# Kernel tuning notes

Measured on AMD Instinct MI355X. Metric: run time of the kernel, lower is better.

Reference implementation:

```python
import jax, jax.numpy as jnp
import numpy as np

NUM_USERS = 100000
NUM_ITEMS = 100000
D = 128
L = 8
FV = 64
FH = 64
B = 8192
FC_IN = FV * D + FH * L  # 8704


def setup_inputs() -> dict:
    key = jax.random.key(0)
    ks = jax.random.split(key, 16)
    s = 0.05  # weight scale for sane magnitudes
    return {
        "user_id": jax.random.randint(ks[0], (B,), 0, NUM_USERS),
        "seq_L": jax.random.randint(ks[1], (B, L), 0, NUM_ITEMS),
        "item_id": jax.random.randint(ks[2], (B,), 0, NUM_ITEMS),
        "Q": jax.random.normal(ks[3], (NUM_ITEMS, D), jnp.float32) * s,
        "P": jax.random.normal(ks[4], (NUM_USERS, D), jnp.float32) * s,
        "Qp": jax.random.normal(ks[5], (NUM_ITEMS, 2 * D), jnp.float32) * s,
        "b_item": jax.random.normal(ks[6], (NUM_ITEMS,), jnp.float32) * s,
        "Wv": jax.random.normal(ks[7], (FV, L), jnp.float32) * s,
        "bv": jax.random.normal(ks[8], (FV,), jnp.float32) * s,
        "Wh": jax.random.normal(ks[9], (L, FH, L, D), jnp.float32) * s,
        "bh": jax.random.normal(ks[10], (L, FH), jnp.float32) * s,
        "Wfc": jax.random.normal(ks[11], (D, FC_IN), jnp.float32) * s,
        "bfc": jax.random.normal(ks[12], (D,), jnp.float32) * s,
    }


def reference(user_id, seq_L, item_id, Q, P, Qp, b_item, Wv, bv, Wh, bh, Wfc, bfc):
    # seq embeddings: [B, L, D]
    x = Q[seq_L]
    # vertical conv: kernel (L,1) -> out [B, Fv, D], then relu + flatten
    out_v = jax.nn.relu(jnp.einsum("bld,fl->bfd", x, Wv) + bv[None, :, None])
    out_v = out_v.reshape(out_v.shape[0], FV * D)  # [B, Fv*D]
    # horizontal conv blocks h = 1..L (static loop over kernel heights)
    h_feats = []
    for h in range(1, L + 1):
        w = Wh[h - 1, :, :h, :]  # [Fh, h, D]
        # sliding windows over sequence: [B, L-h+1, h, D]
        win = jnp.stack([x[:, j : j + h] for j in range(L - h + 1)], axis=1)
        o = jnp.einsum("bjhd,fhd->bjf", win, w) + bh[h - 1]  # [B, L-h+1, Fh]
        h_feats.append(jnp.max(jax.nn.relu(o), axis=1))  # [B, Fh]
    out_h = jnp.concatenate(h_feats, axis=1)  # [B, Fh*L]
    combined = jnp.concatenate([out_v, out_h], axis=1)  # [B, Fv*D + Fh*L]
    # (dropout p=0 / inference -> identity)
    z = jax.nn.relu(combined @ Wfc.T + bfc)  # [B, D]
    x2 = jnp.concatenate([z, P[user_id]], axis=1)  # [B, 2D]
    score = jnp.einsum("bd,bd->b", x2, Qp[item_id]) + b_item[item_id]
    return score
```

## Files before the change

kernel.cpp:

```cpp
#include <hip/hip_runtime.h>
#include <hip/hip_bf16.h>
#include <cstdint>
#include <cstddef>

typedef short bf16x8 __attribute__((ext_vector_type(8)));
typedef short bf16x4 __attribute__((ext_vector_type(4)));
typedef float f32x4  __attribute__((ext_vector_type(4)));

#define MFMA16(A, B, C) __builtin_amdgcn_mfma_f32_16x16x32_bf16(A, B, C, 0, 0, 0)

constexpr int XSTR = 1032;
constexpr int BSTR = 520;
constexpr size_t WS_FC   = (size_t)2176 * 1024;
constexpr size_t WS_BOTH = WS_FC + (size_t)576 * 1024;

__device__ __forceinline__ unsigned short f2bf(float x) {
    unsigned u = __float_as_uint(x);
    unsigned r = u + 0x7fffu + ((u >> 16) & 1u);
    return (unsigned short)(r >> 16);
}
__device__ __forceinline__ float bf2f(unsigned short h) {
    return __uint_as_float(((unsigned)h) << 16);
}
__device__ __forceinline__ unsigned pkbf(float a, float b) {
    __hip_bfloat162 h = __float22bfloat162_rn(make_float2(a, b));
    return *reinterpret_cast<unsigned*>(&h);
}
__device__ __forceinline__ bf16x8 load8_f32(const float* __restrict__ s) {
    float4 a = *(const float4*)s;
    float4 b = *(const float4*)(s + 4);
    bf16x8 r;
    r[0]=(short)f2bf(a.x); r[1]=(short)f2bf(a.y); r[2]=(short)f2bf(a.z); r[3]=(short)f2bf(a.w);
    r[4]=(short)f2bf(b.x); r[5]=(short)f2bf(b.y); r[6]=(short)f2bf(b.z); r[7]=(short)f2bf(b.w);
    return r;
}

template<int MODE>
__device__ __forceinline__ bf16x8 fc_bfrag(const unsigned short* __restrict__ wfcb,
                                           const float* __restrict__ Wfc,
                                           int kg, int ntile, int lane)
{
    if constexpr (MODE >= 1) {
        return *(const bf16x8*)(wfcb + (((size_t)(kg * 8 + ntile)) << 9) + lane * 8);
    } else {
        const float* s = Wfc + (size_t)(ntile * 16 + (lane & 15)) * 8704
                             + kg * 32 + (lane >> 4) * 8;
        return load8_f32(s);
    }
}
template<int MODE>
__device__ __forceinline__ bf16x8 wh_bfrag(const unsigned short* __restrict__ whb,
                                           const float* __restrict__ Wh,
                                           int H, int kstep, int ntile, int lane)
{
    if constexpr (MODE == 2) {
        return *(const bf16x8*)(whb +
            (((size_t)(8 * H * (H - 1) + kstep * 4 + ntile)) << 9) + lane * 8);
    } else {
        const int k = kstep * 32 + (lane >> 4) * 8;
        const float* s = Wh + ((((size_t)(H - 1) * 64 + ntile * 16 + (lane & 15)) * 8
                               + (k >> 7)) * 128 + (k & 127));
        return load8_f32(s);
    }
}

__global__ __launch_bounds__(256)
void caser_prep(const float* __restrict__ Wfc, const float* __restrict__ Wh,
                unsigned short* __restrict__ wfcb, unsigned short* __restrict__ whb,
                int nfrag)
{
    const int tid = blockIdx.x * 256 + threadIdx.x;
    const int lane = tid & 63, frag = tid >> 6;
    if (frag >= nfrag) return;
    if (frag < 2176) {
        const int kg = frag >> 3, nt = frag & 7;
        bf16x8 v = fc_bfrag<0>(nullptr, Wfc, kg, nt, lane);
        *(bf16x8*)(wfcb + ((size_t)frag << 9) + lane * 8) = v;
    } else {
        const int f2 = frag - 2176;
        int h = 1;
        while (f2 >= 8 * h * (h + 1)) ++h;
        const int fl = f2 - 8 * h * (h - 1);
        const int nt = fl & 3, kstep = fl >> 2;
        bf16x8 v = wh_bfrag<0>(nullptr, Wh, h, kstep, nt, lane);
        *(bf16x8*)(whb + ((size_t)f2 << 9) + lane * 8) = v;
    }
}

template<int H, int PP, int MODE>
__device__ __forceinline__ void hconv_compute(
    const unsigned short* __restrict__ xs,
    const unsigned short* __restrict__ whb, const float* __restrict__ Wh,
    const float* __restrict__ bh,
    int m, int nt4, int lane, int laneA, float mx[4])
{
    constexpr int NJ = 9 - H;
    constexpr int NJS = (PP == 0) ? ((NJ + 1) / 2) : (NJ / 2);
    if constexpr (NJS > 0) {
        f32x4 C[NJS] = {};
        const unsigned short* xbase = xs + m * 16 * XSTR + laneA;
        #pragma unroll
        for (int kstep = 0; kstep < 4 * H; ++kstep) {
            const int hp = kstep >> 2, d0 = (kstep & 3) * 32;
            bf16x8 B = wh_bfrag<MODE>(whb, Wh, H, kstep, nt4, lane);
            #pragma unroll
            for (int idx = 0; idx < NJS; ++idx) {
                const int j = PP + 2 * idx;
                bf16x8 A = *(const bf16x8*)(xbase + (j + hp) * 128 + d0);
                C[idx] = MFMA16(A, B, C[idx]);
            }
        }
        const float bhv = bh[(H - 1) * 64 + nt4 * 16 + (lane & 15)];
        #pragma unroll
        for (int idx = 0; idx < NJS; ++idx)
            #pragma unroll
            for (int r = 0; r < 4; ++r)
                mx[r] = fmaxf(mx[r], fmaxf(C[idx][r] + bhv, 0.f));
    }
}

template<int H, int MODE>
__device__ __forceinline__ void hstep(
    const unsigned short* __restrict__ xs, unsigned short* __restrict__ feat,
    float* __restrict__ cand,
    const unsigned short* __restrict__ whb, const float* __restrict__ Wh,
    const float* __restrict__ bh,
    int t, int lane, int laneA, int hm, int hn4, int pj)
{
    float mx[4] = {};
    if (pj == 0) hconv_compute<H, 0, MODE>(xs, whb, Wh, bh, hm, hn4, lane, laneA, mx);
    else         hconv_compute<H, 1, MODE>(xs, whb, Wh, bh, hm, hn4, lane, laneA, mx);
    #pragma unroll
    for (int r = 0; r < 4; ++r)
        cand[pj * 2176 + (hm * 16 + (lane >> 4) * 4 + r) * 68 +
             hn4 * 16 + (lane & 15)] = mx[r];
    __syncthreads();
    {
        const int s = t >> 5, f0 = (t & 31) * 2;
        float a0 = fmaxf(cand[s * 68 + f0],     cand[2176 + s * 68 + f0]);
        float a1 = fmaxf(cand[s * 68 + f0 + 1], cand[2176 + s * 68 + f0 + 1]);
        *(unsigned*)(feat + s * BSTR + (H - 1) * 64 + f0) = pkbf(a0, a1);
    }
    __syncthreads();
}

template<int MODE>
__global__ __launch_bounds__(1024, 1)
void caser_main(const int* __restrict__ user_id,
                const int* __restrict__ seq,
                const int* __restrict__ item_id,
                const float* __restrict__ Q,
                const float* __restrict__ Pmat,
                const float* __restrict__ Qp,
                const float* __restrict__ b_item,
                const float* __restrict__ Wv,
                const float* __restrict__ bv,
                const float* __restrict__ Wh,
                const float* __restrict__ bh,
                const float* __restrict__ Wfc,
                const float* __restrict__ bfc,
                const unsigned short* __restrict__ wfcb,
                const unsigned short* __restrict__ whb,
                float* __restrict__ out)
{
    __shared__ unsigned short xs[32 * XSTR];
    __shared__ unsigned short fbuf[2 * 32 * BSTR];
    __shared__ float cand[2 * 32 * 68];
    __shared__ float wv_s[576];

    const int t = threadIdx.x;
    const int lane = t & 63;
    const int w = t >> 6;
    const int b0 = blockIdx.x * 32;
    const int laneA = (lane & 15) * XSTR + (lane >> 4) * 8;
    const int laneB = (lane & 15) * BSTR + (lane >> 4) * 8;
    const int kh = w & 3, ng = w >> 2;
    const int hm = w & 1, hn4 = (w >> 1) & 3, pj = (w >> 3) & 1;

    if (t < 576) wv_s[t] = (t < 512) ? Wv[t] : bv[t - 512];
    #pragma unroll
    for (int k = 0; k < 8; ++k) {
        const int idx = t + k * 1024;
        const int i = idx & 31;
        const int l = (idx >> 5) & 7;
        const int s = idx >> 8;
        const int it = seq[(b0 + s) * 8 + l];
        float4 v = *(const float4*)(Q + (size_t)it * 128 + i * 4);
        uint2 pk;
        pk.x = pkbf(v.x, v.y);
        pk.y = pkbf(v.z, v.w);
        *(uint2*)(xs + s * XSTR + l * 128 + i * 4) = pk;
    }
    __syncthreads();

    const int sv = t & 31, dq = t >> 5;
    float xr[8][4];
    #pragma unroll
    for (int l = 0; l < 8; ++l) {
        bf16x4 v = *(const bf16x4*)(xs + sv * XSTR + l * 128 + dq * 4);
        #pragma unroll
        for (int i = 0; i < 4; ++i) xr[l][i] = bf2f((unsigned short)v[i]);
    }

    f32x4 FCC[2][2] = {};

    uint2 vc[4];
    #define VCONV_HALF(hc_, dst_)                                              \
        {                                                                      \
            _Pragma("unroll")                                                  \
            for (int fl = 0; fl < 4; ++fl) {                                   \
                const int f = (hc_) * 4 + fl;                                  \
                const float bvv = wv_s[512 + f];                               \
                float acc[4];                                                  \
                _Pragma("unroll")                                              \
                for (int i = 0; i < 4; ++i) acc[i] = bvv;                      \
                _Pragma("unroll")                                              \
                for (int l = 0; l < 8; ++l) {                                  \
                    const float wl = wv_s[f * 8 + l];                          \
                    _Pragma("unroll")                                          \
                    for (int i = 0; i < 4; ++i)                                \
                        acc[i] = fmaf(xr[l][i], wl, acc[i]);                   \
                }                                                              \
                dst_[fl].x = pkbf(fmaxf(acc[0], 0.f), fmaxf(acc[1], 0.f));     \
                dst_[fl].y = pkbf(fmaxf(acc[2], 0.f), fmaxf(acc[3], 0.f));     \
            }                                                                  \
        }
    #define VSTORE(buf_)                                                       \
        {                                                                      \
            unsigned short* fb = fbuf + (buf_) * (32 * BSTR);                  \
            _Pragma("unroll")                                                  \
            for (int fl = 0; fl < 4; ++fl)                                     \
                *(uint2*)(fb + sv * BSTR + fl * 128 + dq * 4) = vc[fl];        \
        }

    VCONV_HALF(0, vc);
    VSTORE(0);
    __syncthreads();

    #pragma unroll 2
    for (int hc = 0; hc < 16; ++hc) {
        uint2 nxt[4];
        if (hc < 15) VCONV_HALF(hc + 1, nxt);
        {
            const unsigned short* fb = fbuf + (hc & 1) * (32 * BSTR);
            #pragma unroll
            for (int ks = 0; ks < 4; ++ks) {
                const int kl = kh * 4 + ks;
                const int kg = hc * 16 + kl;
                bf16x8 B0 = fc_bfrag<MODE>(wfcb, Wfc, kg, ng * 2,     lane);
                bf16x8 B1 = fc_bfrag<MODE>(wfcb, Wfc, kg, ng * 2 + 1, lane);
                bf16x8 A0 = *(const bf16x8*)(fb + laneB + kl * 32);
                bf16x8 A1 = *(const bf16x8*)(fb + 16 * BSTR + laneB + kl * 32);
                FCC[0][0] = MFMA16(A0, B0, FCC[0][0]);
                FCC[0][1] = MFMA16(A0, B1, FCC[0][1]);
                FCC[1][0] = MFMA16(A1, B0, FCC[1][0]);
                FCC[1][1] = MFMA16(A1, B1, FCC[1][1]);
            }
        }
        if (hc < 15) {
            #pragma unroll
            for (int fl = 0; fl < 4; ++fl) vc[fl] = nxt[fl];
            VSTORE((hc + 1) & 1);
        }
        __syncthreads();
    }
    #undef VCONV_HALF
    #undef VSTORE

    unsigned short* feat = fbuf;
    hstep<1, MODE>(xs, feat, cand, whb, Wh, bh, t, lane, laneA, hm, hn4, pj);
    hstep<2, MODE>(xs, feat, cand, whb, Wh, bh, t, lane, laneA, hm, hn4, pj);
    hstep<3, MODE>(xs, feat, cand, whb, Wh, bh, t, lane, laneA, hm, hn4, pj);
    hstep<4, MODE>(xs, feat, cand, whb, Wh, bh, t, lane, laneA, hm, hn4, pj);
    hstep<5, MODE>(xs, feat, cand, whb, Wh, bh, t, lane, laneA, hm, hn4, pj);
    hstep<6, MODE>(xs, feat, cand, whb, Wh, bh, t, lane, laneA, hm, hn4, pj);
    hstep<7, MODE>(xs, feat, cand, whb, Wh, bh, t, lane, laneA, hm, hn4, pj);
    hstep<8, MODE>(xs, feat, cand, whb, Wh, bh, t, lane, laneA, hm, hn4, pj);

    #pragma unroll
    for (int kgi = 0; kgi < 4; ++kgi) {
        const int kloc = kh * 4 + kgi;
        const int kg = 256 + kloc;
        bf16x8 B0 = fc_bfrag<MODE>(wfcb, Wfc, kg, ng * 2,     lane);
        bf16x8 B1 = fc_bfrag<MODE>(wfcb, Wfc, kg, ng * 2 + 1, lane);
        bf16x8 A0 = *(const bf16x8*)(feat + laneB + kloc * 32);
        bf16x8 A1 = *(const bf16x8*)(feat + 16 * BSTR + laneB + kloc * 32);
        FCC[0][0] = MFMA16(A0, B0, FCC[0][0]);
        FCC[0][1] = MFMA16(A0, B1, FCC[0][1]);
        FCC[1][0] = MFMA16(A1, B0, FCC[1][0]);
        FCC[1][1] = MFMA16(A1, B1, FCC[1][1]);
    }

    float* zbuf4 = (float*)xs;
    #pragma unroll
    for (int m = 0; m < 2; ++m)
        #pragma unroll
        for (int nt = 0; nt < 2; ++nt)
            #pragma unroll
            for (int r = 0; r < 4; ++r)
                zbuf4[kh * (32 * 132) + (m * 16 + (lane >> 4) * 4 + r) * 132 +
                      ng * 32 + nt * 16 + (lane & 15)] = FCC[m][nt][r];
    __syncthreads();
    {
        const int s = t >> 5, l32 = t & 31, o0 = l32 * 4;
        const int b = b0 + s;
        const int item = item_id[b];
        const int user = user_id[b];
        const float* qp = Qp + (size_t)item * 256;
        const float* pu = Pmat + (size_t)user * 128;
        float acc2 = 0.f;
        #pragma unroll
        for (int i = 0; i < 4; ++i) {
            float z = zbuf4[s * 132 + o0 + i]
                    + zbuf4[1 * (32 * 132) + s * 132 + o0 + i]
                    + zbuf4[2 * (32 * 132) + s * 132 + o0 + i]
                    + zbuf4[3 * (32 * 132) + s * 132 + o0 + i]
                    + bfc[o0 + i];
            z = fmaxf(z, 0.f);
            acc2 = fmaf(z, qp[o0 + i], acc2);
        }
        #pragma unroll
        for (int i = 0; i < 4; ++i)
            acc2 = fmaf(pu[o0 + i], qp[128 + o0 + i], acc2);
        acc2 += __shfl_xor(acc2, 1, 32);
        acc2 += __shfl_xor(acc2, 2, 32);
        acc2 += __shfl_xor(acc2, 4, 32);
        acc2 += __shfl_xor(acc2, 8, 32);
        acc2 += __shfl_xor(acc2, 16, 32);
        if (l32 == 0) out[b] = acc2 + b_item[item];
    }
}

extern "C" void kernel_launch(void* const* d_in, const int* in_sizes, int n_in,
                              void* d_out, int out_size, void* d_ws, size_t ws_size,
                              hipStream_t stream)
{
    const int*   user_id = (const int*)  d_in[0];
    const int*   seq     = (const int*)  d_in[1];
    const int*   item_id = (const int*)  d_in[2];
    const float* Q       = (const float*)d_in[3];
    const float* Pmat    = (const float*)d_in[4];
    const float* Qp      = (const float*)d_in[5];
    const float* b_item  = (const float*)d_in[6];
    const float* Wv      = (const float*)d_in[7];
    const float* bv      = (const float*)d_in[8];
    const float* Wh      = (const float*)d_in[9];
    const float* bh      = (const float*)d_in[10];
    const float* Wfc     = (const float*)d_in[11];
    const float* bfc     = (const float*)d_in[12];
    float* out = (float*)d_out;

    unsigned short* wfcb = (unsigned short*)d_ws;
    unsigned short* whb  = wfcb + WS_FC / 2;

    if (ws_size >= WS_BOTH) {
        hipLaunchKernelGGL(caser_prep, dim3(688), dim3(256), 0, stream,
                           Wfc, Wh, wfcb, whb, 2752);
        hipLaunchKernelGGL((caser_main<2>), dim3(256), dim3(1024), 0, stream,
                           user_id, seq, item_id, Q, Pmat, Qp, b_item,
                           Wv, bv, Wh, bh, Wfc, bfc, wfcb, whb, out);
    } else if (ws_size >= WS_FC) {
        hipLaunchKernelGGL(caser_prep, dim3(544), dim3(256), 0, stream,
                           Wfc, Wh, wfcb, whb, 2176);
        hipLaunchKernelGGL((caser_main<1>), dim3(256), dim3(1024), 0, stream,
                           user_id, seq, item_id, Q, Pmat, Qp, b_item,
                           Wv, bv, Wh, bh, Wfc, bfc, wfcb, whb, out);
    } else {
        hipLaunchKernelGGL((caser_main<0>), dim3(256), dim3(1024), 0, stream,
                           user_id, seq, item_id, Q, Pmat, Qp, b_item,
                           Wv, bv, Wh, bh, Wfc, bfc,
                           (const unsigned short*)nullptr, (const unsigned short*)nullptr, out);
    }
}
```

Baseline: 85.87 us.

## Prefetch FC weight fragments a chunk ahead and double-buffer hconv candidate buffers

FC weight B-fragments are now loaded into registers one chunk ahead of their use, so their global latency overlaps the current chunk's MFMAs instead of stalling them. The vertical conv for the next chunk moves after the MFMAs, and the loop unroll drops to 1. The horizontal conv steps alternate between two candidate buffers, which removes one barrier per step, and the tail FC fragment loads are issued before the final sync. This raises register pressure and reuses part of fbuf as scratch, which is only safe if the lifetimes of those regions do not overlap.

```diff
diff --git a/kernel.cpp b/kernel.cpp
--- a/kernel.cpp
+++ b/kernel.cpp
@@ -122,7 +122,7 @@
 template<int H, int MODE>
 __device__ __forceinline__ void hstep(
     const unsigned short* __restrict__ xs, unsigned short* __restrict__ feat,
-    float* __restrict__ cand,
+    float* __restrict__ candc,
     const unsigned short* __restrict__ whb, const float* __restrict__ Wh,
     const float* __restrict__ bh,
     int t, int lane, int laneA, int hm, int hn4, int pj)
@@ -132,16 +132,15 @@
     else         hconv_compute<H, 1, MODE>(xs, whb, Wh, bh, hm, hn4, lane, laneA, mx);
     #pragma unroll
     for (int r = 0; r < 4; ++r)
-        cand[pj * 2176 + (hm * 16 + (lane >> 4) * 4 + r) * 68 +
-             hn4 * 16 + (lane & 15)] = mx[r];
+        candc[pj * 2176 + (hm * 16 + (lane >> 4) * 4 + r) * 68 +
+              hn4 * 16 + (lane & 15)] = mx[r];
     __syncthreads();
     {
         const int s = t >> 5, f0 = (t & 31) * 2;
-        float a0 = fmaxf(cand[s * 68 + f0],     cand[2176 + s * 68 + f0]);
-        float a1 = fmaxf(cand[s * 68 + f0 + 1], cand[2176 + s * 68 + f0 + 1]);
+        float a0 = fmaxf(candc[s * 68 + f0],     candc[2176 + s * 68 + f0]);
+        float a1 = fmaxf(candc[s * 68 + f0 + 1], candc[2176 + s * 68 + f0 + 1]);
         *(unsigned*)(feat + s * BSTR + (H - 1) * 64 + f0) = pkbf(a0, a1);
     }
-    __syncthreads();
 }
 
 template<int MODE>
@@ -205,7 +204,7 @@
     f32x4 FCC[2][2] = {};
 
     uint2 vc[4];
-    #define VCONV_HALF(hc_, dst_)                                              \
+    #define VCONV_HALF(hc_)                                                    \
         {                                                                      \
             _Pragma("unroll")                                                  \
             for (int fl = 0; fl < 4; ++fl) {                                   \
@@ -221,8 +220,8 @@
                     for (int i = 0; i < 4; ++i)                                \
                         acc[i] = fmaf(xr[l][i], wl, acc[i]);                   \
                 }                                                              \
-                dst_[fl].x = pkbf(fmaxf(acc[0], 0.f), fmaxf(acc[1], 0.f));     \
-                dst_[fl].y = pkbf(fmaxf(acc[2], 0.f), fmaxf(acc[3], 0.f));     \
+                vc[fl].x = pkbf(fmaxf(acc[0], 0.f), fmaxf(acc[1], 0.f));       \
+                vc[fl].y = pkbf(fmaxf(acc[2], 0.f), fmaxf(acc[3], 0.f));       \
             }                                                                  \
         }
     #define VSTORE(buf_)                                                       \
@@ -233,33 +232,40 @@
                 *(uint2*)(fb + sv * BSTR + fl * 128 + dq * 4) = vc[fl];        \
         }
 
-    VCONV_HALF(0, vc);
+    bf16x8 BF0[4], BF1[4];
+    #pragma unroll
+    for (int ks = 0; ks < 4; ++ks) {
+        const int kg = kh * 4 + ks;
+        BF0[ks] = fc_bfrag<MODE>(wfcb, Wfc, kg, ng * 2,     lane);
+        BF1[ks] = fc_bfrag<MODE>(wfcb, Wfc, kg, ng * 2 + 1, lane);
+    }
+    VCONV_HALF(0);
     VSTORE(0);
     __syncthreads();
 
-    #pragma unroll 2
+    #pragma unroll 1
     for (int hc = 0; hc < 16; ++hc) {
-        uint2 nxt[4];
-        if (hc < 15) VCONV_HALF(hc + 1, nxt);
         {
             const unsigned short* fb = fbuf + (hc & 1) * (32 * BSTR);
             #pragma unroll
             for (int ks = 0; ks < 4; ++ks) {
                 const int kl = kh * 4 + ks;
-                const int kg = hc * 16 + kl;
-                bf16x8 B0 = fc_bfrag<MODE>(wfcb, Wfc, kg, ng * 2,     lane);
-                bf16x8 B1 = fc_bfrag<MODE>(wfcb, Wfc, kg, ng * 2 + 1, lane);
                 bf16x8 A0 = *(const bf16x8*)(fb + laneB + kl * 32);
                 bf16x8 A1 = *(const bf16x8*)(fb + 16 * BSTR + laneB + kl * 32);
-                FCC[0][0] = MFMA16(A0, B0, FCC[0][0]);
-                FCC[0][1] = MFMA16(A0, B1, FCC[0][1]);
-                FCC[1][0] = MFMA16(A1, B0, FCC[1][0]);
-                FCC[1][1] = MFMA16(A1, B1, FCC[1][1]);
+                FCC[0][0] = MFMA16(A0, BF0[ks], FCC[0][0]);
+                FCC[0][1] = MFMA16(A0, BF1[ks], FCC[0][1]);
+                FCC[1][0] = MFMA16(A1, BF0[ks], FCC[1][0]);
+                FCC[1][1] = MFMA16(A1, BF1[ks], FCC[1][1]);
             }
         }
         if (hc < 15) {
             #pragma unroll
-            for (int fl = 0; fl < 4; ++fl) vc[fl] = nxt[fl];
+            for (int ks = 0; ks < 4; ++ks) {
+                const int kg = (hc + 1) * 16 + kh * 4 + ks;
+                BF0[ks] = fc_bfrag<MODE>(wfcb, Wfc, kg, ng * 2,     lane);
+                BF1[ks] = fc_bfrag<MODE>(wfcb, Wfc, kg, ng * 2 + 1, lane);
+            }
+            VCONV_HALF(hc + 1);
             VSTORE((hc + 1) & 1);
         }
         __syncthreads();
@@ -268,27 +274,34 @@
     #undef VSTORE
 
     unsigned short* feat = fbuf;
-    hstep<1, MODE>(xs, feat, cand, whb, Wh, bh, t, lane, laneA, hm, hn4, pj);
-    hstep<2, MODE>(xs, feat, cand, whb, Wh, bh, t, lane, laneA, hm, hn4, pj);
-    hstep<3, MODE>(xs, feat, cand, whb, Wh, bh, t, lane, laneA, hm, hn4, pj);
-    hstep<4, MODE>(xs, feat, cand, whb, Wh, bh, t, lane, laneA, hm, hn4, pj);
-    hstep<5, MODE>(xs, feat, cand, whb, Wh, bh, t, lane, laneA, hm, hn4, pj);
-    hstep<6, MODE>(xs, feat, cand, whb, Wh, bh, t, lane, laneA, hm, hn4, pj);
-    hstep<7, MODE>(xs, feat, cand, whb, Wh, bh, t, lane, laneA, hm, hn4, pj);
-    hstep<8, MODE>(xs, feat, cand, whb, Wh, bh, t, lane, laneA, hm, hn4, pj);
+    float* candA = cand;
+    float* candB = (float*)(fbuf + 32 * BSTR);
+    hstep<1, MODE>(xs, feat, candA, whb, Wh, bh, t, lane, laneA, hm, hn4, pj);
+    hstep<2, MODE>(xs, feat, candB, whb, Wh, bh, t, lane, laneA, hm, hn4, pj);
+    hstep<3, MODE>(xs, feat, candA, whb, Wh, bh, t, lane, laneA, hm, hn4, pj);
+    hstep<4, MODE>(xs, feat, candB, whb, Wh, bh, t, lane, laneA, hm, hn4, pj);
+    hstep<5, MODE>(xs, feat, candA, whb, Wh, bh, t, lane, laneA, hm, hn4, pj);
+    hstep<6, MODE>(xs, feat, candB, whb, Wh, bh, t, lane, laneA, hm, hn4, pj);
+    hstep<7, MODE>(xs, feat, candA, whb, Wh, bh, t, lane, laneA, hm, hn4, pj);
+    hstep<8, MODE>(xs, feat, candB, whb, Wh, bh, t, lane, laneA, hm, hn4, pj);
+
+    #pragma unroll
+    for (int kgi = 0; kgi < 4; ++kgi) {
+        const int kg = 256 + kh * 4 + kgi;
+        BF0[kgi] = fc_bfrag<MODE>(wfcb, Wfc, kg, ng * 2,     lane);
+        BF1[kgi] = fc_bfrag<MODE>(wfcb, Wfc, kg, ng * 2 + 1, lane);
+    }
+    __syncthreads();
 
     #pragma unroll
     for (int kgi = 0; kgi < 4; ++kgi) {
         const int kloc = kh * 4 + kgi;
-        const int kg = 256 + kloc;
-        bf16x8 B0 = fc_bfrag<MODE>(wfcb, Wfc, kg, ng * 2,     lane);
-        bf16x8 B1 = fc_bfrag<MODE>(wfcb, Wfc, kg, ng * 2 + 1, lane);
         bf16x8 A0 = *(const bf16x8*)(feat + laneB + kloc * 32);
         bf16x8 A1 = *(const bf16x8*)(feat + 16 * BSTR + laneB + kloc * 32);
-        FCC[0][0] = MFMA16(A0, B0, FCC[0][0]);
-        FCC[0][1] = MFMA16(A0, B1, FCC[0][1]);
-        FCC[1][0] = MFMA16(A1, B0, FCC[1][0]);
-        FCC[1][1] = MFMA16(A1, B1, FCC[1][1]);
+        FCC[0][0] = MFMA16(A0, BF0[kgi], FCC[0][0]);
+        FCC[0][1] = MFMA16(A0, BF1[kgi], FCC[0][1]);
+        FCC[1][0] = MFMA16(A1, BF0[kgi], FCC[1][0]);
+        FCC[1][1] = MFMA16(A1, BF1[kgi], FCC[1][1]);
     }
 
     float* zbuf4 = (float*)xs;
```

Result: faster. 78.44 us (-8.7%).
